# Performance work log

Hardware: AMD Instinct MI355X
Metric: run time of the kernel (lower is better)

Reference implementation:

```python
import jax, jax.numpy as jnp
import numpy as np

N = 30000  # nodes per type (drug and protein)


def graph_conv(x, s, d, W, b):
    # DGL GraphConv, norm='both': h = D_in^{-1/2} A (D_out^{-1/2} x) W + b
    ones = jnp.ones(s.shape, dtype=x.dtype)
    deg_out = jnp.maximum(jax.ops.segment_sum(ones, s, num_segments=N), 1.0)
    deg_in = jnp.maximum(jax.ops.segment_sum(ones, d, num_segments=N), 1.0)
    xh = (x * deg_out[:, None] ** -0.5) @ W          # transform first (in > out)
    agg = jax.ops.segment_sum(xh[s], d, num_segments=N)  # gather-scatter over edges
    return agg * deg_in[:, None] ** -0.5 + b


def rgcn_channel(xd, xp, src_c, dst_c, W1c, b1c, W2c, b2c):
    # relations: 0 drug->drug, 1 drug->protein, 2 protein->drug, 3 protein->protein
    hd = jax.nn.relu(graph_conv(xd, src_c[0], dst_c[0], W1c[0], b1c[0])
                     + graph_conv(xp, src_c[2], dst_c[2], W1c[2], b1c[2]))
    hp = jax.nn.relu(graph_conv(xd, src_c[1], dst_c[1], W1c[1], b1c[1])
                     + graph_conv(xp, src_c[3], dst_c[3], W1c[3], b1c[3]))
    hd2 = jax.nn.relu(graph_conv(hd, src_c[0], dst_c[0], W2c[0], b2c[0])
                      + graph_conv(hp, src_c[2], dst_c[2], W2c[2], b2c[2]))
    hp2 = jax.nn.relu(graph_conv(hd, src_c[1], dst_c[1], W2c[1], b2c[1])
                      + graph_conv(hp, src_c[3], dst_c[3], W2c[3], b2c[3]))
    return hd2, hp2


def semantic_attention(z, Wp, bp, q):
    # z: [N, K, F] -> beta [K], emb [N, F]
    w = jnp.tanh(z @ Wp + bp) @ q            # [N, K]
    beta = jax.nn.softmax(jnp.mean(w, axis=0))  # [K]
    return beta, jnp.einsum('k,nkf->nf', beta, z)


def setup_inputs() -> dict:
    key = jax.random.key(0)
    ks = jax.random.split(key, 8)
    E = 250000
    in_f, hid_f, out_f = 512, 256, 128
    x_drug = jax.random.normal(ks[0], (N, in_f), dtype=jnp.float32)
    x_pro = jax.random.normal(ks[1], (N, in_f), dtype=jnp.float32)
    src = jax.random.randint(ks[2], (4, 4, E), 0, N, dtype=jnp.int32)
    dst = jax.random.randint(ks[3], (4, 4, E), 0, N, dtype=jnp.int32)
    W1 = jax.random.normal(ks[4], (4, 4, in_f, hid_f), dtype=jnp.float32) / np.sqrt(in_f)
    b1 = jnp.zeros((4, 4, hid_f), dtype=jnp.float32)
    W2 = jax.random.normal(ks[5], (4, 4, hid_f, out_f), dtype=jnp.float32) / np.sqrt(hid_f)
    b2 = jnp.zeros((4, 4, out_f), dtype=jnp.float32)
    Wp = jax.random.normal(ks[6], (out_f, out_f), dtype=jnp.float32) / np.sqrt(out_f)
    bp = jnp.zeros((out_f,), dtype=jnp.float32)
    q = jax.random.normal(ks[7], (out_f,), dtype=jnp.float32) / np.sqrt(out_f)
    return {"x_drug": x_drug, "x_pro": x_pro, "src": src, "dst": dst,
            "W1": W1, "b1": b1, "W2": W2, "b2": b2, "Wp": Wp, "bp": bp, "q": q}


def reference(x_drug, x_pro, src, dst, W1, b1, W2, b2, Wp, bp, q):
    h_drug, h_pro = [], []
    for c in range(4):  # 4 channel graphs (fixed small loop)
        hd, hp = rgcn_channel(x_drug, x_pro, src[c], dst[c], W1[c], b1[c], W2[c], b2[c])
        h_drug.append(hd)
        h_pro.append(hp)
    # MCKRL stacks channels 0, 2, 3 only
    z_drug = jnp.stack([h_drug[0], h_drug[2], h_drug[3]], axis=1)  # [N,3,F]
    z_pro = jnp.stack([h_pro[0], h_pro[2], h_pro[3]], axis=1)
    beta_drug, emb_drug = semantic_attention(z_drug, Wp, bp, q)
    beta_pro, emb_pro = semantic_attention(z_pro, Wp, bp, q)
    return emb_drug, emb_pro, beta_drug, beta_pro
```

## Files before the change

kernel.cpp:

```cpp
#include <hip/hip_runtime.h>
#include <math.h>


#define IN_F  512
#define HID_F 256
#define OUT_F 128
#define NG    12
#define NPART 16
#define RANGE 1875
#define ES    8

typedef _Float16 f16x2 __attribute__((ext_vector_type(2)));
typedef _Float16 f16x8 __attribute__((ext_vector_type(8)));
typedef float    f32x4 __attribute__((ext_vector_type(4)));

#define AS1 __attribute__((address_space(1)))
#define AS3 __attribute__((address_space(3)))

__device__ __forceinline__ void gld16(const void* g, void* l) {
    __builtin_amdgcn_global_load_lds((const AS1 void*)g, (AS3 void*)l, 16, 0, 0);
}

__host__ __device__ __forceinline__ int chan_of(int ci) { return ci == 0 ? 0 : ci + 1; }

__global__ __launch_bounds__(512) void k_hist(const int* __restrict__ src,
                                              const int* __restrict__ dst,
                                              int* __restrict__ hin,
                                              int* __restrict__ hout,
                                              int N, int E) {
    __shared__ int hi[RANGE], ho[RANGE];
    int g = blockIdx.x, p = blockIdx.y, es = blockIdx.z, t = threadIdx.x;
    for (int i = t; i < RANGE; i += 512) { hi[i] = 0; ho[i] = 0; }
    __syncthreads();
    int ci = g >> 2, c = chan_of(ci), r = g & 3;
    const int* sp = src + (size_t)(c * 4 + r) * E;
    const int* dp = dst + (size_t)(c * 4 + r) * E;
    int lo = p * RANGE;
    int sl = E / ES;
    int e0 = es * sl, e1 = (es == ES - 1) ? E : e0 + sl;
    for (int e = e0 + t; e < e1; e += 512) {
        int s = sp[e] - lo;
        int d = dp[e] - lo;
        if ((unsigned)s < (unsigned)RANGE) atomicAdd(&ho[s], 1);
        if ((unsigned)d < (unsigned)RANGE) atomicAdd(&hi[d], 1);
    }
    __syncthreads();
    int* hing  = hin  + ((size_t)g * ES + es) * N;
    int* houtg = hout + ((size_t)g * ES + es) * N;
    for (int i = t; i < RANGE; i += 512) {
        int node = lo + i;
        if (node < N) { hing[node] = hi[i]; houtg[node] = ho[i]; }
    }
}

__global__ void k_rs2(const int* __restrict__ hin, const int* __restrict__ hout,
                      int* __restrict__ deg_in,
                      float* __restrict__ rs_out, float* __restrict__ rs_in, int N) {
    int i = blockIdx.x * 256 + threadIdx.x;
    if (i >= NG * N) return;
    int g = i / N, n = i - g * N;
    int di = 0, dq = 0;
#pragma unroll
    for (int es = 0; es < ES; ++es) {
        di += hin [((size_t)g * ES + es) * N + n];
        dq += hout[((size_t)g * ES + es) * N + n];
    }
    deg_in[i] = di;
    rs_in[i]  = rsqrtf(fmaxf((float)di, 1.0f));
    rs_out[i] = rsqrtf(fmaxf((float)dq, 1.0f));
}

__global__ __launch_bounds__(1024) void k_scan(const int* __restrict__ deg_in,
                                               int* __restrict__ row_ptr, int N) {
    int g = blockIdx.x;
    const int* dg = deg_in + (size_t)g * N;
    int* rp = row_ptr + (size_t)g * (N + 1);
    __shared__ int wsum[16];
    int tid = threadIdx.x;
    int lane = tid & 63, wv = tid >> 6;
    int run = 0;
    for (int basei = 0; basei < N; basei += 1024) {
        int i = basei + tid;
        int v = (i < N) ? dg[i] : 0;
        int x = v;
#pragma unroll
        for (int off = 1; off < 64; off <<= 1) {
            int y = __shfl_up(x, off);
            if (lane >= off) x += y;
        }
        if (lane == 63) wsum[wv] = x;
        __syncthreads();
        if (wv == 0) {
            int s = (lane < 16) ? wsum[lane] : 0;
#pragma unroll
            for (int off = 1; off < 16; off <<= 1) {
                int y = __shfl_up(s, off);
                if (lane >= off) s += y;
            }
            if (lane < 16) wsum[lane] = s;
        }
        __syncthreads();
        int woff = wv ? wsum[wv - 1] : 0;
        if (i < N) rp[i] = run + woff + x - v;
        run += wsum[15];
        __syncthreads();
    }
    if (tid == 0) rp[N] = run;
}

__global__ __launch_bounds__(512) void k_fill3(const int* __restrict__ src,
                                               const int* __restrict__ dst,
                                               const int* __restrict__ row_ptr,
                                               const int* __restrict__ hin,
                                               int* __restrict__ col, int N, int E) {
    __shared__ int cur[RANGE];
    int g = blockIdx.x, p = blockIdx.y, es = blockIdx.z, t = threadIdx.x;
    int lo = p * RANGE;
    const int* rp = row_ptr + (size_t)g * (N + 1);
    for (int i = t; i < RANGE; i += 512) {
        int node = lo + i;
        int base = 0;
        if (node < N) {
            base = rp[node];
            for (int e2 = 0; e2 < es; ++e2)
                base += hin[((size_t)g * ES + e2) * N + node];
        }
        cur[i] = base;
    }
    __syncthreads();
    int ci = g >> 2, c = chan_of(ci), r = g & 3;
    const int* sp = src + (size_t)(c * 4 + r) * E;
    const int* dp = dst + (size_t)(c * 4 + r) * E;
    int* cg = col + (size_t)g * E;
    int sl = E / ES;
    int e0 = es * sl, e1 = (es == ES - 1) ? E : e0 + sl;
    for (int e = e0 + t; e < e1; e += 512) {
        int s = sp[e];
        int d = dp[e] - lo;
        if ((unsigned)d < (unsigned)RANGE) {
            int pos = atomicAdd(&cur[d], 1);
            cg[pos] = s;
        }
    }
}

__global__ void k_cvt16(const float* __restrict__ in, _Float16* __restrict__ out,
                        size_t n) {
    size_t i = ((size_t)blockIdx.x * 256 + threadIdx.x) * 8;
    if (i >= n) return;
    float4 a = *(const float4*)(in + i);
    float4 b = *(const float4*)(in + i + 4);
    f16x8 v;
    v[0] = (_Float16)a.x; v[1] = (_Float16)a.y; v[2] = (_Float16)a.z; v[3] = (_Float16)a.w;
    v[4] = (_Float16)b.x; v[5] = (_Float16)b.y; v[6] = (_Float16)b.z; v[7] = (_Float16)b.w;
    *(f16x8*)(out + i) = v;
}

__global__ __launch_bounds__(256) void k_cvtT(const float* __restrict__ W,
                                              _Float16* __restrict__ out,
                                              int K, int Nn) {
    __shared__ float tile[32][33];
    int gi = blockIdx.z, ci = gi >> 2, c = chan_of(ci), r = gi & 3;
    const float* Wg = W + (size_t)(c * 4 + r) * K * Nn;
    _Float16* Wo = out + ((size_t)(ci * 2 + (r >> 1)) * 2 * Nn + (size_t)(r & 1) * Nn) * K;
    int k0 = blockIdx.x * 32, n0 = blockIdx.y * 32;
    int tx = threadIdx.x & 31, ty = threadIdx.x >> 5;
    for (int yy = ty; yy < 32; yy += 8)
        tile[yy][tx] = Wg[(size_t)(k0 + yy) * Nn + n0 + tx];
    __syncthreads();
    for (int yy = ty; yy < 32; yy += 8)
        Wo[(size_t)(n0 + yy) * K + k0 + tx] = (_Float16)tile[tx][yy];
}

__global__ __launch_bounds__(256) void k_cvtWp(const float* __restrict__ Wp,
                                               _Float16* __restrict__ WpT) {
    __shared__ float tile[32][33];
    int k0 = blockIdx.x * 32, n0 = blockIdx.y * 32;
    int tx = threadIdx.x & 31, ty = threadIdx.x >> 5;
    for (int yy = ty; yy < 32; yy += 8)
        tile[yy][tx] = Wp[(size_t)(k0 + yy) * 128 + n0 + tx];
    __syncthreads();
    for (int yy = ty; yy < 32; yy += 8)
        WpT[(size_t)(n0 + yy) * 128 + k0 + tx] = (_Float16)tile[tx][yy];
}

__global__ __launch_bounds__(256) void k_gemm16(const _Float16* __restrict__ A0, size_t Azs,
                                                const _Float16* __restrict__ B0, size_t Bzs,
                                                _Float16* __restrict__ C0, size_t Czs,
                                                int M, int K, int Nn) {
    const _Float16* A = A0 + (size_t)blockIdx.z * Azs;
    const _Float16* Bt = B0 + (size_t)blockIdx.z * Bzs;
    _Float16* C = C0 + (size_t)blockIdx.z * Czs;
    __shared__ __align__(16) _Float16 As[128 * 64];
    __shared__ __align__(16) _Float16 Bs[128 * 64];
    int t = threadIdx.x;
    int lane = t & 63, wid = t >> 6;
    int wm = wid >> 1, wn = wid & 1;
    int brow = blockIdx.y * 128, bcol = blockIdx.x * 128;

    f32x4 acc[4][4] = {};
    int mrow = lane & 15;
    int khalf = lane >> 4;

    for (int k0 = 0; k0 < K; k0 += 64) {
        __syncthreads();
#pragma unroll
        for (int i = 0; i < 4; ++i) {
            int L = t + i * 256;
            int row = L >> 3, spp = L & 7;
            int sg = spp ^ (row & 7);
            int ra = brow + row; if (ra > M - 1) ra = M - 1;
            gld16((const void*)(A + (size_t)ra * K + (size_t)(k0 + sg * 8)),
                  (void*)(As + (size_t)(i * 256 + wid * 64) * 8));
            int rb = bcol + row;
            gld16((const void*)(Bt + (size_t)rb * K + (size_t)(k0 + sg * 8)),
                  (void*)(Bs + (size_t)(i * 256 + wid * 64) * 8));
        }
        __syncthreads();
#pragma unroll
        for (int ks = 0; ks < 2; ++ks) {
            f16x8 af[4], bf[4];
#pragma unroll
            for (int mi = 0; mi < 4; ++mi) {
                int r = wm * 64 + mi * 16 + mrow;
                int s = ks * 4 + khalf;
                int ph = s ^ (r & 7);
                af[mi] = *(const f16x8*)(As + r * 64 + ph * 8);
            }
#pragma unroll
            for (int ni = 0; ni < 4; ++ni) {
                int r = wn * 64 + ni * 16 + mrow;
                int s = ks * 4 + khalf;
                int ph = s ^ (r & 7);
                bf[ni] = *(const f16x8*)(Bs + r * 64 + ph * 8);
            }
#pragma unroll
            for (int mi = 0; mi < 4; ++mi)
#pragma unroll
                for (int ni = 0; ni < 4; ++ni)
                    acc[mi][ni] = __builtin_amdgcn_mfma_f32_16x16x32_f16(
                        af[mi], bf[ni], acc[mi][ni], 0, 0, 0);
        }
    }
#pragma unroll
    for (int mi = 0; mi < 4; ++mi) {
#pragma unroll
        for (int r = 0; r < 4; ++r) {
            int row = brow + wm * 64 + mi * 16 + (lane >> 4) * 4 + r;
            if (row < M) {
#pragma unroll
                for (int ni = 0; ni < 4; ++ni) {
                    int colx = bcol + wn * 64 + ni * 16 + (lane & 15);
                    C[(size_t)row * Nn + colx] = (_Float16)acc[mi][ni][r];
                }
            }
        }
    }
}

__global__ void k_agg2(const _Float16* __restrict__ Ya0, const _Float16* __restrict__ Yb0,
                       int ystride,
                       const int* __restrict__ row_ptr, const int* __restrict__ col,
                       const float* __restrict__ rs_out, const float* __restrict__ rs_in,
                       int ga0, int gb0,
                       const float* __restrict__ ba0, const float* __restrict__ bb0,
                       _Float16* __restrict__ outb, size_t out_sidestride, int ostride,
                       int F, int N, int E) {
    int i = blockIdx.x, side = blockIdx.y;
    int f0 = 2 * threadIdx.x;
    const _Float16* Ya = Ya0 + side * F;
    const _Float16* Yb = Yb0 + side * F;
    int ga = ga0 + side, gb = gb0 + side;
    float a0 = ba0[side * F + f0] + bb0[side * F + f0];
    float a1 = ba0[side * F + f0 + 1] + bb0[side * F + f0 + 1];
    {
        const int* rp = row_ptr + (size_t)ga * (N + 1);
        const int* cg = col + (size_t)ga * E;
        const float* ro = rs_out + (size_t)ga * N;
        int beg = rp[i], end = rp[i + 1];
        float s0 = 0.0f, s1 = 0.0f;
        int sn = (beg < end) ? cg[beg] : 0;
        for (int e = beg; e < end; ++e) {
            int sn1 = (e + 1 < end) ? cg[e + 1] : 0;
            f16x2 v = *(const f16x2*)(Ya + (size_t)sn * ystride + f0);
            float w = ro[sn];
            s0 = fmaf(w, (float)v[0], s0);
            s1 = fmaf(w, (float)v[1], s1);
            sn = sn1;
        }
        float ri = rs_in[(size_t)ga * N + i];
        a0 = fmaf(ri, s0, a0); a1 = fmaf(ri, s1, a1);
    }
    {
        const int* rp = row_ptr + (size_t)gb * (N + 1);
        const int* cg = col + (size_t)gb * E;
        const float* ro = rs_out + (size_t)gb * N;
        int beg = rp[i], end = rp[i + 1];
        float s0 = 0.0f, s1 = 0.0f;
        int sn = (beg < end) ? cg[beg] : 0;
        for (int e = beg; e < end; ++e) {
            int sn1 = (e + 1 < end) ? cg[e + 1] : 0;
            f16x2 v = *(const f16x2*)(Yb + (size_t)sn * ystride + f0);
            float w = ro[sn];
            s0 = fmaf(w, (float)v[0], s0);
            s1 = fmaf(w, (float)v[1], s1);
            sn = sn1;
        }
        float ri = rs_in[(size_t)gb * N + i];
        a0 = fmaf(ri, s0, a0); a1 = fmaf(ri, s1, a1);
    }
    f16x2 o;
    o[0] = (_Float16)fmaxf(a0, 0.0f);
    o[1] = (_Float16)fmaxf(a1, 0.0f);
    *(f16x2*)(outb + side * out_sidestride + (size_t)i * ostride + f0) = o;
}

__global__ __launch_bounds__(256) void k_wred(const _Float16* __restrict__ T,
                                              const float* __restrict__ bp,
                                              const float* __restrict__ q,
                                              float* __restrict__ w_all, int N) {
    int m = blockIdx.x * 4 + (threadIdx.x >> 6);
    int lane = threadIdx.x & 63;
    if (m >= 6 * N) return;
    f16x2 v2 = *(const f16x2*)(T + (size_t)m * 128 + 2 * lane);
    float v = tanhf((float)v2[0] + bp[2 * lane]) * q[2 * lane]
            + tanhf((float)v2[1] + bp[2 * lane + 1]) * q[2 * lane + 1];
#pragma unroll
    for (int o = 1; o < 64; o <<= 1) v += __shfl_xor(v, o);
    if (lane == 0) {
        int side = m / (3 * N);
        int rem = m - side * 3 * N;
        int node = rem / 3, k = rem - node * 3;
        w_all[((size_t)side * 3 + k) * N + node] = v;
    }
}

__global__ __launch_bounds__(256) void k_beta(const float* __restrict__ w_all,
                                              float* __restrict__ beta_ws,
                                              float* __restrict__ beta_out, int N) {
    int side = blockIdx.x;
    int tid = threadIdx.x;
    __shared__ float red[256];
    float sums[3];
    for (int k = 0; k < 3; ++k) {
        float s = 0.0f;
        for (int i = tid; i < N; i += 256) s += w_all[((size_t)side * 3 + k) * N + i];
        red[tid] = s;
        __syncthreads();
        for (int off = 128; off > 0; off >>= 1) {
            if (tid < off) red[tid] += red[tid + off];
            __syncthreads();
        }
        sums[k] = red[0];
        __syncthreads();
    }
    if (tid == 0) {
        float inv = 1.0f / (float)N;
        float m0 = sums[0] * inv, m1 = sums[1] * inv, m2 = sums[2] * inv;
        float mx = fmaxf(m0, fmaxf(m1, m2));
        float e0 = expf(m0 - mx), e1 = expf(m1 - mx), e2 = expf(m2 - mx);
        float denom = e0 + e1 + e2;
        float b0 = e0 / denom, b1 = e1 / denom, b2 = e2 / denom;
        beta_ws[side * 3 + 0] = b0; beta_out[side * 3 + 0] = b0;
        beta_ws[side * 3 + 1] = b1; beta_out[side * 3 + 1] = b1;
        beta_ws[side * 3 + 2] = b2; beta_out[side * 3 + 2] = b2;
    }
}

__global__ __launch_bounds__(64) void k_emb(const _Float16* __restrict__ z,
                                            const float* __restrict__ beta_ws,
                                            float* __restrict__ out, int N) {
    int i = blockIdx.x, side = blockIdx.y, t = threadIdx.x;
    const _Float16* zr = z + (size_t)side * N * 384 + (size_t)i * 384;
    const float* b = beta_ws + side * 3;
    f16x2 z0 = *(const f16x2*)(zr + 2 * t);
    f16x2 z1 = *(const f16x2*)(zr + 128 + 2 * t);
    f16x2 z2 = *(const f16x2*)(zr + 256 + 2 * t);
    float2 o;
    o.x = b[0] * (float)z0[0] + b[1] * (float)z1[0] + b[2] * (float)z2[0];
    o.y = b[0] * (float)z0[1] + b[1] * (float)z1[1] + b[2] * (float)z2[1];
    *(float2*)&out[(size_t)side * N * 128 + (size_t)i * 128 + 2 * t] = o;
}

extern "C" void kernel_launch(void* const* d_in, const int* in_sizes, int n_in,
                              void* d_out, int out_size, void* d_ws, size_t ws_size,
                              hipStream_t stream) {
    const float* x_drug = (const float*)d_in[0];
    const float* x_pro  = (const float*)d_in[1];
    const int*   src    = (const int*)d_in[2];
    const int*   dst    = (const int*)d_in[3];
    const float* W1     = (const float*)d_in[4];
    const float* b1     = (const float*)d_in[5];
    const float* W2     = (const float*)d_in[6];
    const float* b2     = (const float*)d_in[7];
    const float* Wp     = (const float*)d_in[8];
    const float* bp     = (const float*)d_in[9];
    const float* q      = (const float*)d_in[10];
    float* out = (float*)d_out;

    const int N = in_sizes[0] / IN_F;
    const int E = in_sizes[2] / 16;

    size_t off = 0;
    auto alloc = [&](size_t bytes) -> void* {
        void* p = (char*)d_ws + off;
        off += (bytes + 255) & ~(size_t)255;
        return p;
    };
    int*      deg_in  = (int*)alloc((size_t)NG * N * 4);
    int*      row_ptr = (int*)alloc((size_t)NG * (N + 1) * 4);
    int*      col     = (int*)alloc((size_t)NG * E * 4);
    float*    rs_out  = (float*)alloc((size_t)NG * N * 4);
    float*    rs_in   = (float*)alloc((size_t)NG * N * 4);
    _Float16* xh      = (_Float16*)alloc((size_t)2 * N * IN_F * 2);
    _Float16* W1cat   = (_Float16*)alloc((size_t)6 * 2 * HID_F * IN_F * 2);
    _Float16* W2cat   = (_Float16*)alloc((size_t)6 * 2 * OUT_F * HID_F * 2);
    _Float16* WpT     = (_Float16*)alloc((size_t)128 * 128 * 2);
    _Float16* Y1      = (_Float16*)alloc((size_t)2 * N * 512 * 2);
    _Float16* Y2      = (_Float16*)alloc((size_t)2 * N * 256 * 2);
    _Float16* H1      = (_Float16*)alloc((size_t)2 * N * HID_F * 2);
    _Float16* zbuf    = (_Float16*)alloc((size_t)2 * N * 384 * 2);
    float*    w_all   = (float*)alloc((size_t)2 * 3 * N * 4);
    float*    beta_ws = (float*)alloc(64);
    int*      hin  = (int*)Y1;
    int*      hout = hin + (size_t)NG * ES * N;
    _Float16* T    = Y1;
    (void)ws_size; (void)n_in; (void)out_size;

    dim3 hg(NG, NPART, ES);
    k_hist<<<hg, 512, 0, stream>>>(src, dst, hin, hout, N, E);
    k_rs2<<<(NG * N + 255) / 256, 256, 0, stream>>>(hin, hout, deg_in, rs_out, rs_in, N);
    k_scan<<<NG, 1024, 0, stream>>>(deg_in, row_ptr, N);
    k_fill3<<<hg, 512, 0, stream>>>(src, dst, row_ptr, hin, col, N, E);

    size_t nx = (size_t)N * IN_F;
    k_cvt16<<<(int)((nx / 8 + 255) / 256), 256, 0, stream>>>(x_drug, xh, nx);
    k_cvt16<<<(int)((nx / 8 + 255) / 256), 256, 0, stream>>>(x_pro,  xh + nx, nx);
    k_cvtT<<<dim3(IN_F / 32, HID_F / 32, NG), 256, 0, stream>>>(W1, W1cat, IN_F, HID_F);
    k_cvtT<<<dim3(HID_F / 32, OUT_F / 32, NG), 256, 0, stream>>>(W2, W2cat, HID_F, OUT_F);
    k_cvtWp<<<dim3(4, 4), 256, 0, stream>>>(Wp, WpT);

    dim3 g1(512 / 128, (N + 127) / 128, 2);
    dim3 g2(256 / 128, (N + 127) / 128, 2);
    dim3 agrid(N, 2);

    for (int ci = 0; ci < 3; ++ci) {
        int c = chan_of(ci);
        k_gemm16<<<g1, 256, 0, stream>>>(xh, (size_t)N * IN_F,
                                         W1cat + (size_t)ci * 2 * 512 * 512, (size_t)512 * 512,
                                         Y1, (size_t)N * 512,
                                         N, IN_F, 512);
        k_agg2<<<agrid, HID_F / 2, 0, stream>>>(Y1, Y1 + (size_t)N * 512, 512,
                                                row_ptr, col, rs_out, rs_in,
                                                ci * 4 + 0, ci * 4 + 2,
                                                b1 + (size_t)c * 4 * HID_F, b1 + (size_t)(c * 4 + 2) * HID_F,
                                                H1, (size_t)N * HID_F, HID_F, HID_F, N, E);
        k_gemm16<<<g2, 256, 0, stream>>>(H1, (size_t)N * HID_F,
                                         W2cat + (size_t)ci * 2 * 256 * 256, (size_t)256 * 256,
                                         Y2, (size_t)N * 256,
                                         N, HID_F, 256);
        k_agg2<<<agrid, OUT_F / 2, 0, stream>>>(Y2, Y2 + (size_t)N * 256, 256,
                                                row_ptr, col, rs_out, rs_in,
                                                ci * 4 + 0, ci * 4 + 2,
                                                b2 + (size_t)c * 4 * OUT_F, b2 + (size_t)(c * 4 + 2) * OUT_F,
                                                zbuf + (size_t)ci * OUT_F, (size_t)N * 384, 384, OUT_F, N, E);
    }

    int Mrows = 2 * N * 3;
    dim3 gT(1, (Mrows + 127) / 128, 1);
    k_gemm16<<<gT, 256, 0, stream>>>(zbuf, 0, WpT, 0, T, 0, Mrows, 128, 128);
    k_wred<<<(Mrows + 3) / 4, 256, 0, stream>>>(T, bp, q, w_all, N);
    k_beta<<<2, 256, 0, stream>>>(w_all, beta_ws, out + (size_t)2 * N * OUT_F, N);
    k_emb<<<agrid, 64, 0, stream>>>(zbuf, beta_ws, out, N);
}
```

Baseline: 1.374 ms.

## Fold out-degree scaling into GEMM epilogue and vectorize wave-per-node aggregation

Moves the D_out^{-1/2} source scaling from the per-edge aggregation loop into the GEMM epilogue, scaled per row and per relation half via Nsplit. The aggregation kernels now assign one 64-lane wave per destination node with 4- or 2-wide fp16 vectors, and unroll edges by 4 with masked duplicate loads. This removes the per-edge rs_out gather and the tiny 64/128-thread blocks, and exposes more independent loads per lane. In exchange the scale is applied before the fp16 rounding of the GEMM output rather than after, and the masked tail iterations issue redundant loads.

```diff
diff --git a/kernel.cpp b/kernel.cpp
--- a/kernel.cpp
+++ b/kernel.cpp
@@ -11,6 +11,7 @@
 #define ES    8
 
 typedef _Float16 f16x2 __attribute__((ext_vector_type(2)));
+typedef _Float16 f16x4 __attribute__((ext_vector_type(4)));
 typedef _Float16 f16x8 __attribute__((ext_vector_type(8)));
 typedef float    f32x4 __attribute__((ext_vector_type(4)));
 
@@ -187,10 +188,13 @@
 __global__ __launch_bounds__(256) void k_gemm16(const _Float16* __restrict__ A0, size_t Azs,
                                                 const _Float16* __restrict__ B0, size_t Bzs,
                                                 _Float16* __restrict__ C0, size_t Czs,
+                                                const float* __restrict__ rs0, int rsN,
+                                                int Nsplit,
                                                 int M, int K, int Nn) {
     const _Float16* A = A0 + (size_t)blockIdx.z * Azs;
     const _Float16* Bt = B0 + (size_t)blockIdx.z * Bzs;
     _Float16* C = C0 + (size_t)blockIdx.z * Czs;
+    const float* rsA = rs0 ? rs0 + (size_t)(2 * blockIdx.z) * rsN : nullptr;
     __shared__ __align__(16) _Float16 As[128 * 64];
     __shared__ __align__(16) _Float16 Bs[128 * 64];
     int t = threadIdx.x;
@@ -248,71 +252,113 @@
         for (int r = 0; r < 4; ++r) {
             int row = brow + wm * 64 + mi * 16 + (lane >> 4) * 4 + r;
             if (row < M) {
+                float sA = 1.0f, sB = 1.0f;
+                if (rsA) { sA = rsA[row]; sB = rsA[rsN + row]; }
 #pragma unroll
                 for (int ni = 0; ni < 4; ++ni) {
                     int colx = bcol + wn * 64 + ni * 16 + (lane & 15);
-                    C[(size_t)row * Nn + colx] = (_Float16)acc[mi][ni][r];
+                    float sc = (colx < Nsplit) ? sA : sB;
+                    C[(size_t)row * Nn + colx] = (_Float16)(acc[mi][ni][r] * sc);
                 }
             }
         }
     }
 }
 
-__global__ void k_agg2(const _Float16* __restrict__ Ya0, const _Float16* __restrict__ Yb0,
-                       int ystride,
-                       const int* __restrict__ row_ptr, const int* __restrict__ col,
-                       const float* __restrict__ rs_out, const float* __restrict__ rs_in,
-                       int ga0, int gb0,
-                       const float* __restrict__ ba0, const float* __restrict__ bb0,
-                       _Float16* __restrict__ outb, size_t out_sidestride, int ostride,
-                       int F, int N, int E) {
-    int i = blockIdx.x, side = blockIdx.y;
-    int f0 = 2 * threadIdx.x;
+template<typename FV, int VEC>
+__device__ __forceinline__ void agg_body(const _Float16* __restrict__ Ya0,
+                                         const _Float16* __restrict__ Yb0, int ystride,
+                                         const int* __restrict__ row_ptr,
+                                         const int* __restrict__ col,
+                                         const float* __restrict__ rs_in,
+                                         int ga0, int gb0,
+                                         const float* __restrict__ ba0,
+                                         const float* __restrict__ bb0,
+                                         _Float16* __restrict__ outb,
+                                         size_t out_sidestride, int ostride,
+                                         int F, int N, int E) {
+    int wv = threadIdx.x >> 6, lane = threadIdx.x & 63;
+    int i = blockIdx.x * 4 + wv;
+    if (i >= N) return;
+    int side = blockIdx.y;
+    int f0 = VEC * lane;
     const _Float16* Ya = Ya0 + side * F;
     const _Float16* Yb = Yb0 + side * F;
     int ga = ga0 + side, gb = gb0 + side;
-    float a0 = ba0[side * F + f0] + bb0[side * F + f0];
-    float a1 = ba0[side * F + f0 + 1] + bb0[side * F + f0 + 1];
+
+    float accA[VEC] = {}, accB[VEC] = {};
     {
         const int* rp = row_ptr + (size_t)ga * (N + 1);
         const int* cg = col + (size_t)ga * E;
-        const float* ro = rs_out + (size_t)ga * N;
         int beg = rp[i], end = rp[i + 1];
-        float s0 = 0.0f, s1 = 0.0f;
-        int sn = (beg < end) ? cg[beg] : 0;
-        for (int e = beg; e < end; ++e) {
-            int sn1 = (e + 1 < end) ? cg[e + 1] : 0;
-            f16x2 v = *(const f16x2*)(Ya + (size_t)sn * ystride + f0);
-            float w = ro[sn];
-            s0 = fmaf(w, (float)v[0], s0);
-            s1 = fmaf(w, (float)v[1], s1);
-            sn = sn1;
-        }
-        float ri = rs_in[(size_t)ga * N + i];
-        a0 = fmaf(ri, s0, a0); a1 = fmaf(ri, s1, a1);
+        for (int e = beg; e < end; e += 4) {
+            int s0 = cg[e];
+            bool b1 = e + 1 < end, b2 = e + 2 < end, b3 = e + 3 < end;
+            int s1 = b1 ? cg[e + 1] : s0;
+            int s2 = b2 ? cg[e + 2] : s0;
+            int s3 = b3 ? cg[e + 3] : s0;
+            FV v0 = *(const FV*)(Ya + (size_t)s0 * ystride + f0);
+            FV v1 = *(const FV*)(Ya + (size_t)s1 * ystride + f0);
+            FV v2 = *(const FV*)(Ya + (size_t)s2 * ystride + f0);
+            FV v3 = *(const FV*)(Ya + (size_t)s3 * ystride + f0);
+            float m1 = b1 ? 1.0f : 0.0f, m2 = b2 ? 1.0f : 0.0f, m3 = b3 ? 1.0f : 0.0f;
+#pragma unroll
+            for (int k = 0; k < VEC; ++k)
+                accA[k] += (float)v0[k] + m1 * (float)v1[k]
+                         + m2 * (float)v2[k] + m3 * (float)v3[k];
+        }
     }
     {
         const int* rp = row_ptr + (size_t)gb * (N + 1);
         const int* cg = col + (size_t)gb * E;
-        const float* ro = rs_out + (size_t)gb * N;
         int beg = rp[i], end = rp[i + 1];
-        float s0 = 0.0f, s1 = 0.0f;
-        int sn = (beg < end) ? cg[beg] : 0;
-        for (int e = beg; e < end; ++e) {
-            int sn1 = (e + 1 < end) ? cg[e + 1] : 0;
-            f16x2 v = *(const f16x2*)(Yb + (size_t)sn * ystride + f0);
-            float w = ro[sn];
-            s0 = fmaf(w, (float)v[0], s0);
-            s1 = fmaf(w, (float)v[1], s1);
-            sn = sn1;
-        }
-        float ri = rs_in[(size_t)gb * N + i];
-        a0 = fmaf(ri, s0, a0); a1 = fmaf(ri, s1, a1);
-    }
-    f16x2 o;
-    o[0] = (_Float16)fmaxf(a0, 0.0f);
-    o[1] = (_Float16)fmaxf(a1, 0.0f);
-    *(f16x2*)(outb + side * out_sidestride + (size_t)i * ostride + f0) = o;
+        for (int e = beg; e < end; e += 4) {
+            int s0 = cg[e];
+            bool b1 = e + 1 < end, b2 = e + 2 < end, b3 = e + 3 < end;
+            int s1 = b1 ? cg[e + 1] : s0;
+            int s2 = b2 ? cg[e + 2] : s0;
+            int s3 = b3 ? cg[e + 3] : s0;
+            FV v0 = *(const FV*)(Yb + (size_t)s0 * ystride + f0);
+            FV v1 = *(const FV*)(Yb + (size_t)s1 * ystride + f0);
+            FV v2 = *(const FV*)(Yb + (size_t)s2 * ystride + f0);
+            FV v3 = *(const FV*)(Yb + (size_t)s3 * ystride + f0);
+            float m1 = b1 ? 1.0f : 0.0f, m2 = b2 ? 1.0f : 0.0f, m3 = b3 ? 1.0f : 0.0f;
+#pragma unroll
+            for (int k = 0; k < VEC; ++k)
+                accB[k] += (float)v0[k] + m1 * (float)v1[k]
+                         + m2 * (float)v2[k] + m3 * (float)v3[k];
+        }
+    }
+    float ria = rs_in[(size_t)ga * N + i];
+    float rib = rs_in[(size_t)gb * N + i];
+    FV o;
+#pragma unroll
+    for (int k = 0; k < VEC; ++k) {
+        float v = ria * accA[k] + rib * accB[k]
+                + ba0[side * F + f0 + k] + bb0[side * F + f0 + k];
+        o[k] = (_Float16)fmaxf(v, 0.0f);
+    }
+    *(FV*)(outb + side * out_sidestride + (size_t)i * ostride + f0) = o;
+}
+
+__global__ __launch_bounds__(256) void k_agg256(const _Float16* Ya0, const _Float16* Yb0,
+                                                int ystride, const int* row_ptr, const int* col,
+                                                const float* rs_in, int ga0, int gb0,
+                                                const float* ba0, const float* bb0,
+                                                _Float16* outb, size_t oss, int ostride,
+                                                int N, int E) {
+    agg_body<f16x4, 4>(Ya0, Yb0, ystride, row_ptr, col, rs_in, ga0, gb0,
+                       ba0, bb0, outb, oss, ostride, 256, N, E);
+}
+
+__global__ __launch_bounds__(256) void k_agg128(const _Float16* Ya0, const _Float16* Yb0,
+                                                int ystride, const int* row_ptr, const int* col,
+                                                const float* rs_in, int ga0, int gb0,
+                                                const float* ba0, const float* bb0,
+                                                _Float16* outb, size_t oss, int ostride,
+                                                int N, int E) {
+    agg_body<f16x2, 2>(Ya0, Yb0, ystride, row_ptr, col, rs_in, ga0, gb0,
+                       ba0, bb0, outb, oss, ostride, 128, N, E);
 }
 
 __global__ __launch_bounds__(256) void k_wred(const _Float16* __restrict__ T,
@@ -442,34 +488,38 @@
 
     dim3 g1(512 / 128, (N + 127) / 128, 2);
     dim3 g2(256 / 128, (N + 127) / 128, 2);
-    dim3 agrid(N, 2);
+    dim3 agrid((N + 3) / 4, 2);
+    dim3 egrid(N, 2);
 
     for (int ci = 0; ci < 3; ++ci) {
         int c = chan_of(ci);
         k_gemm16<<<g1, 256, 0, stream>>>(xh, (size_t)N * IN_F,
                                          W1cat + (size_t)ci * 2 * 512 * 512, (size_t)512 * 512,
                                          Y1, (size_t)N * 512,
+                                         rs_out + (size_t)ci * 4 * N, N, 256,
                                          N, IN_F, 512);
-        k_agg2<<<agrid, HID_F / 2, 0, stream>>>(Y1, Y1 + (size_t)N * 512, 512,
-                                                row_ptr, col, rs_out, rs_in,
-                                                ci * 4 + 0, ci * 4 + 2,
-                                                b1 + (size_t)c * 4 * HID_F, b1 + (size_t)(c * 4 + 2) * HID_F,
-                                                H1, (size_t)N * HID_F, HID_F, HID_F, N, E);
+        k_agg256<<<agrid, 256, 0, stream>>>(Y1, Y1 + (size_t)N * 512, 512,
+                                            row_ptr, col, rs_in,
+                                            ci * 4 + 0, ci * 4 + 2,
+                                            b1 + (size_t)c * 4 * HID_F, b1 + (size_t)(c * 4 + 2) * HID_F,
+                                            H1, (size_t)N * HID_F, HID_F, N, E);
         k_gemm16<<<g2, 256, 0, stream>>>(H1, (size_t)N * HID_F,
                                          W2cat + (size_t)ci * 2 * 256 * 256, (size_t)256 * 256,
                                          Y2, (size_t)N * 256,
+                                         rs_out + (size_t)ci * 4 * N, N, 128,
                                          N, HID_F, 256);
-        k_agg2<<<agrid, OUT_F / 2, 0, stream>>>(Y2, Y2 + (size_t)N * 256, 256,
-                                                row_ptr, col, rs_out, rs_in,
-                                                ci * 4 + 0, ci * 4 + 2,
-                                                b2 + (size_t)c * 4 * OUT_F, b2 + (size_t)(c * 4 + 2) * OUT_F,
-                                                zbuf + (size_t)ci * OUT_F, (size_t)N * 384, 384, OUT_F, N, E);
+        k_agg128<<<agrid, 256, 0, stream>>>(Y2, Y2 + (size_t)N * 256, 256,
+                                            row_ptr, col, rs_in,
+                                            ci * 4 + 0, ci * 4 + 2,
+                                            b2 + (size_t)c * 4 * OUT_F, b2 + (size_t)(c * 4 + 2) * OUT_F,
+                                            zbuf + (size_t)ci * OUT_F, (size_t)N * 384, 384, N, E);
     }
 
     int Mrows = 2 * N * 3;
     dim3 gT(1, (Mrows + 127) / 128, 1);
-    k_gemm16<<<gT, 256, 0, stream>>>(zbuf, 0, WpT, 0, T, 0, Mrows, 128, 128);
+    k_gemm16<<<gT, 256, 0, stream>>>(zbuf, 0, WpT, 0, T, 0,
+                                     nullptr, 0, 0, Mrows, 128, 128);
     k_wred<<<(Mrows + 3) / 4, 256, 0, stream>>>(T, bp, q, w_all, N);
     k_beta<<<2, 256, 0, stream>>>(w_all, beta_ws, out + (size_t)2 * N * OUT_F, N);
-    k_emb<<<agrid, 64, 0, stream>>>(zbuf, beta_ws, out, N);
-}
+    k_emb<<<egrid, 64, 0, stream>>>(zbuf, beta_ws, out, N);
+}
```

After: 1.216 ms. 1.13x faster.
